# Kernel tuning notes

Measured on AMD Instinct MI355X. Metric: run time of the kernel, lower is better.

The kernel has to match this reference:

```python
import jax, jax.numpy as jnp
import numpy as np

B, N, CIN, COUT, K, L, NNZ = 4, 4096, 128, 128, 10, 50, 65536


def _spmm(idx, vals, X):
    # COO spmm: out[r] += vals * X[c]; idx: [2, nnz], X: [N, F]
    rows, cols = idx[0], idx[1]
    return jax.ops.segment_sum(vals[:, None] * X[cols], rows, num_segments=N)

_bspmm = jax.vmap(_spmm, in_axes=(0, 0, 0))  # batched over leading dim


def _hgnn_layer(phi_idx, phi_val, inv_idx, inv_val, fea, W, d):
    # original: ((phi @ diag(d)) @ phi_inv) @ (fea @ W)
    # identical math, evaluated right-to-left to stay sparse-dense only
    filt = jnp.einsum('bnc,co->bno', fea, W)            # [B,N,COUT]
    y = _bspmm(inv_idx, inv_val, filt)                  # phi_inv @ X
    y = d[None, :, None] * y                            # diag(d) @ .
    return _bspmm(phi_idx, phi_val, y)                  # phi @ .


def setup_inputs() -> dict:
    key = jax.random.key(0)
    ks = jax.random.split(key, 20)

    def coo(ki, kv):
        idx = jax.random.randint(ki, (B, 2, NNZ), 0, N, dtype=jnp.int32)
        val = jax.random.normal(kv, (B, NNZ), jnp.float32) * 0.05
        return idx, val

    phi1_idx, phi1_val = coo(ks[0], ks[1])
    phi1_inv_idx, phi1_inv_val = coo(ks[2], ks[3])
    phi2_idx, phi2_val = coo(ks[4], ks[5])
    phi2_inv_idx, phi2_inv_val = coo(ks[6], ks[7])
    fea = jax.random.normal(ks[8], (B, N, CIN), jnp.float32)
    joblst = jax.random.randint(ks[9], (B, L), 0, N, dtype=jnp.int64)

    xavier = float(np.sqrt(6.0 / (CIN + COUT)))
    W1 = jax.random.uniform(ks[10], (CIN, COUT), jnp.float32, -xavier, xavier)
    W2 = jax.random.uniform(ks[11], (CIN, COUT), jnp.float32, -xavier, xavier)
    d1 = jax.random.uniform(ks[12], (N,), jnp.float32, 0.9, 1.1)
    d2 = jax.random.uniform(ks[13], (N,), jnp.float32, 0.9, 1.1)
    s = float(1.0 / np.sqrt(N))
    W_ih = jax.random.uniform(ks[14], (N, COUT), jnp.float32, -s, s)
    W_hh = jax.random.uniform(ks[15], (N, N), jnp.float32, -s, s)
    b_ih = jax.random.uniform(ks[16], (N,), jnp.float32, -s, s)
    b_hh = jnp.zeros((N,), jnp.float32)
    sd = float(1.0 / np.sqrt(COUT))
    dense_W = jax.random.uniform(ks[17], (K, COUT), jnp.float32, -sd, sd)
    dense_b = jnp.zeros((K,), jnp.float32)
    item_emb = jax.random.normal(ks[18], (N, COUT), jnp.float32) * 0.01

    return dict(phi1_idx=phi1_idx, phi1_val=phi1_val, phi1_inv_idx=phi1_inv_idx,
                phi1_inv_val=phi1_inv_val, phi2_idx=phi2_idx, phi2_val=phi2_val,
                phi2_inv_idx=phi2_inv_idx, phi2_inv_val=phi2_inv_val,
                fea=fea, joblst=joblst, W1=W1, d1=d1, W2=W2, d2=d2,
                W_ih=W_ih, W_hh=W_hh, b_ih=b_ih, b_hh=b_hh,
                dense_W=dense_W, dense_b=dense_b, item_emb=item_emb)


def reference(phi1_idx, phi1_val, phi1_inv_idx, phi1_inv_val,
              phi2_idx, phi2_val, phi2_inv_idx, phi2_inv_val,
              fea, joblst, W1, d1, W2, d2, W_ih, W_hh, b_ih, b_hh,
              dense_W, dense_b, item_emb):
    # two hypergraph conv layers, summed
    out1 = _hgnn_layer(phi1_idx, phi1_val, phi1_inv_idx, phi1_inv_val, fea, W1, d1)
    out2 = _hgnn_layer(phi2_idx, phi2_val, phi2_inv_idx, phi2_inv_val, fea, W2, d2)
    res = out1 + out2                                   # [B,N,COUT]

    # RNN over job history embeddings (all joblst entries valid -> no -1 filter)
    xs = jnp.swapaxes(item_emb[joblst], 0, 1)           # [L,B,COUT]
    h0 = jnp.zeros((fea.shape[0], N), fea.dtype)

    def step(h, x):
        h = jnp.tanh(x @ W_ih.T + h @ W_hh.T + b_ih + b_hh)
        return h, None

    Emb, _ = jax.lax.scan(step, h0, xs)                 # last hidden: [B,N]

    res2 = jax.nn.gelu(jnp.einsum('bno,ko->bnk', res, dense_W) + dense_b,
                       approximate=False)               # [B,N,K]
    # (res3 * Emb2).permute back == res2 * gelu(Emb) broadcast over K
    return jax.nn.sigmoid(res2 * jax.nn.gelu(Emb, approximate=False)[:, :, None])
```

## Files before the change

### kernel.cpp

```cpp
#include <hip/hip_runtime.h>
#include <cstdint>
#include <cstddef>

#define NN   4096
#define LLC  50

__device__ __forceinline__ float bf2f(unsigned short u) {
    return __uint_as_float(((unsigned)u) << 16);
}
__device__ __forceinline__ unsigned short f2bf(float x) {
    unsigned b = __float_as_uint(x);
    return (unsigned short)((b + 0x7fffu + ((b >> 16) & 1u)) >> 16);
}

#if __has_builtin(__builtin_amdgcn_sdot4)
#define SDOT4(a, b, c) __builtin_amdgcn_sdot4((int)(a), (int)(b), (c), false)
#else
__device__ __forceinline__ int sdot4_sw(unsigned a, unsigned b, int c) {
    c += (int)(signed char)(a) * (int)(signed char)(b);
    c += (int)(signed char)(a >> 8) * (int)(signed char)(b >> 8);
    c += (int)(signed char)(a >> 16) * (int)(signed char)(b >> 16);
    c += (int)(signed char)(a >> 24) * (int)(signed char)(b >> 24);
    return c;
}
#define SDOT4(a, b, c) sdot4_sw((a), (b), (c))
#endif

#define DPPADD(v, ctrl, rmask) \
    ((v) + __builtin_amdgcn_update_dpp(0, (v), (ctrl), (rmask), 0xf, true))
__device__ __forceinline__ int wred64(int v) {
    v = DPPADD(v, 0x111, 0xf);
    v = DPPADD(v, 0x112, 0xf);
    v = DPPADD(v, 0x114, 0xf);
    v = DPPADD(v, 0x118, 0xf);
    v = DPPADD(v, 0x142, 0xa);
    v = DPPADD(v, 0x143, 0xc);
    return v;
}

__global__ __launch_bounds__(128) void k_filt(const float* __restrict__ fea,
                                              const float* __restrict__ W1,
                                              const float* __restrict__ W2,
                                              unsigned short* __restrict__ f1,
                                              unsigned short* __restrict__ f2) {
    __shared__ float sfea[16][128];
    int t = threadIdx.x;
    int rb = blockIdx.x * 16;
    for (int r = 0; r < 16; ++r) sfea[r][t] = fea[(size_t)(rb + r) * 128 + t];
    __syncthreads();
    float a1[16], a2[16];
#pragma unroll
    for (int r = 0; r < 16; ++r) { a1[r] = 0.f; a2[r] = 0.f; }
    for (int c = 0; c < 128; c += 4) {
        float w10 = W1[(c + 0) * 128 + t], w11 = W1[(c + 1) * 128 + t];
        float w12 = W1[(c + 2) * 128 + t], w13 = W1[(c + 3) * 128 + t];
        float w20 = W2[(c + 0) * 128 + t], w21 = W2[(c + 1) * 128 + t];
        float w22 = W2[(c + 2) * 128 + t], w23 = W2[(c + 3) * 128 + t];
#pragma unroll
        for (int r = 0; r < 16; ++r) {
            float4 f = *(const float4*)&sfea[r][c];
            a1[r] += f.x * w10 + f.y * w11 + f.z * w12 + f.w * w13;
            a2[r] += f.x * w20 + f.y * w21 + f.z * w22 + f.w * w23;
        }
    }
#pragma unroll
    for (int r = 0; r < 16; ++r) {
        f1[(size_t)(rb + r) * 128 + t] = f2bf(a1[r]);
        f2[(size_t)(rb + r) * 128 + t] = f2bf(a2[r]);
    }
}

__global__ __launch_bounds__(256) void k_hist(const int* __restrict__ i0, const int* __restrict__ i1,
                                              const int* __restrict__ i2, const int* __restrict__ i3,
                                              int* __restrict__ counts) {
    __shared__ int lc[4096];
    int t = threadIdx.x;
#pragma unroll
    for (int i = 0; i < 16; ++i) lc[t + i * 256] = 0;
    __syncthreads();
    unsigned blk = blockIdx.x;
    unsigned s = blk >> 4, ch = blk & 15;
    unsigned m = s >> 2, b = s & 3;
    const int* ip = (m == 0) ? i0 : (m == 1) ? i1 : (m == 2) ? i2 : i3;
    unsigned base = b * 131072u + ch * 4096u;
#pragma unroll
    for (int i = 0; i < 16; ++i) {
        int r = ip[base + t + i * 256];
        atomicAdd(&lc[r], 1);
    }
    __syncthreads();
    int* cs = counts + s * 4096;
#pragma unroll
    for (int i = 0; i < 16; ++i) {
        int v = lc[t + i * 256];
        if (v) atomicAdd(cs + t + i * 256, v);
    }
}

__global__ __launch_bounds__(256) void k_scan(const int* __restrict__ counts,
                                              int* __restrict__ rowptr,
                                              int* __restrict__ cursor) {
    int s = blockIdx.x, t = threadIdx.x;
    int loc[16];
    int base = t * 16;
    const int* cs = counts + s * 4096;
    int run = 0;
#pragma unroll
    for (int i = 0; i < 16; ++i) { loc[i] = run; run += cs[base + i]; }
    int total = run;
    int lane = t & 63, wv = t >> 6;
    int v = total;
#pragma unroll
    for (int d = 1; d < 64; d <<= 1) { int u = __shfl_up(v, d, 64); if (lane >= d) v += u; }
    __shared__ int wt[4];
    if (lane == 63) wt[wv] = v;
    __syncthreads();
    int pre = v - total;
    for (int i = 0; i < wv; ++i) pre += wt[i];
    int* rp = rowptr + s * 4097;
    int* cu = cursor + s * 4096;
#pragma unroll
    for (int i = 0; i < 16; ++i) { rp[base + i] = pre + loc[i]; cu[base + i] = pre + loc[i]; }
    if (t == 255) rp[4096] = pre + total;
}

__global__ __launch_bounds__(256) void k_scatter(const int* __restrict__ i0, const int* __restrict__ i1,
                                                 const int* __restrict__ i2, const int* __restrict__ i3,
                                                 const float* __restrict__ v0, const float* __restrict__ v1,
                                                 const float* __restrict__ v2, const float* __restrict__ v3,
                                                 const float* __restrict__ d1, const float* __restrict__ d2,
                                                 int* __restrict__ cursor,
                                                 unsigned* __restrict__ ep) {
    unsigned gid = blockIdx.x * 256 + threadIdx.x;
    unsigned s = gid >> 16, e = gid & 65535;
    unsigned m = s >> 2, b = s & 3;
    const int* ip = (m == 0) ? i0 : (m == 1) ? i1 : (m == 2) ? i2 : i3;
    const float* vp = (m == 0) ? v0 : (m == 1) ? v1 : (m == 2) ? v2 : v3;
    int r = ip[(size_t)b * 131072 + e];
    int c = ip[(size_t)b * 131072 + 65536 + e];
    float v = vp[(size_t)b * 65536 + e];
    if (m == 1) v *= d1[c];
    if (m == 3) v *= d2[c];
    int pos = atomicAdd(cursor + s * 4096 + r, 1);
    ep[(size_t)s * 65536 + pos] = ((unsigned)c << 16) | (unsigned)f2bf(v);
}

__global__ __launch_bounds__(256) void k_xproj(const float* __restrict__ item_emb,
                                               const int* __restrict__ joblst,
                                               const float* __restrict__ W_ih,
                                               const float* __restrict__ b_ih,
                                               const float* __restrict__ b_hh,
                                               float* __restrict__ xp) {
    __shared__ float sx[8][128];
    int t = threadIdx.x;
    int n = blockIdx.x * 256 + t;
    int p0 = blockIdx.y * 8;
#pragma unroll
    for (int i = 0; i < 4; ++i) {
        int e2 = t + i * 256;
        int rr = e2 >> 7, c = e2 & 127;
        int p = p0 + rr;
        int b = p & 3, l = p >> 2;
        int j = joblst[b * LLC + l];
        sx[rr][c] = item_emb[(size_t)j * 128 + c];
    }
    __syncthreads();
    float acc[8];
#pragma unroll
    for (int r = 0; r < 8; ++r) acc[r] = 0.f;
    const float* wn = W_ih + (size_t)n * 128;
    for (int c = 0; c < 128; c += 4) {
        float4 w = *(const float4*)(wn + c);
#pragma unroll
        for (int r = 0; r < 8; ++r) {
            float4 xr = *(const float4*)&sx[r][c];
            acc[r] += xr.x * w.x + xr.y * w.y + xr.z * w.z + xr.w * w.w;
        }
    }
    float bias = b_ih[n] + b_hh[n];
#pragma unroll
    for (int r = 0; r < 8; ++r) xp[(size_t)(p0 + r) * NN + n] = acc[r] + bias;
}

__device__ __forceinline__ void row_acc(const unsigned* __restrict__ eps, int e0, int e1,
                                        const unsigned* __restrict__ Xd, unsigned bbase,
                                        unsigned lane, float& a0, float& a1) {
    int e = e0;
    for (; e + 8 <= e1; e += 8) {
        unsigned p[8], x[8];
#pragma unroll
        for (int i = 0; i < 8; ++i) p[i] = eps[e + i];
#pragma unroll
        for (int i = 0; i < 8; ++i)
            x[i] = Xd[((size_t)(bbase + (p[i] >> 16)) << 6) + lane];
#pragma unroll
        for (int i = 0; i < 8; ++i) {
            float v = bf2f((unsigned short)p[i]);
            a0 += v * bf2f((unsigned short)x[i]);
            a1 += v * bf2f((unsigned short)(x[i] >> 16));
        }
    }
    for (; e < e1; ++e) {
        unsigned pp = eps[e];
        unsigned xw = Xd[((size_t)(bbase + (pp >> 16)) << 6) + lane];
        float v = bf2f((unsigned short)pp);
        a0 += v * bf2f((unsigned short)xw);
        a1 += v * bf2f((unsigned short)(xw >> 16));
    }
}

__global__ __launch_bounds__(256, 2) void k_mega(
        const float* __restrict__ W_hh,
        const float* __restrict__ xp,
        unsigned* __restrict__ hq,
        float* __restrict__ hfin,
        int* __restrict__ bar,
        const int* __restrict__ rowptr,
        const unsigned* __restrict__ ep,
        const unsigned short* __restrict__ filt1,
        const unsigned short* __restrict__ filt2,
        unsigned short* __restrict__ y1,
        unsigned short* __restrict__ y2,
        const float* __restrict__ dW,
        const float* __restrict__ db,
        float* __restrict__ g1) {
    __shared__ unsigned hs[4352];
    __shared__ int red[4][16];
    __shared__ unsigned char hpk[4][4][4];
    int t = threadIdx.x;
    int lane = t & 63, wv = t >> 6;
    int blk = blockIdx.x;

    if (blk >= 256) {
        int w = blk - 256;
        int c7 = w & 7;
        {
            unsigned mm = c7 & 1, b = (unsigned)c7 >> 1;
            int s = (mm ? 8 : 0) + (int)b;
            const unsigned* Xd = (const unsigned*)(mm ? filt2 : filt1);
            unsigned* Yd = (unsigned*)(mm ? y2 : y1);
            const int* rp = rowptr + s * 4097;
            const unsigned* eps = ep + (size_t)s * 65536;
            unsigned bbase = b * 4096;
            int g = w >> 3;
            int row0 = (g * 4 + wv) * 16;
            for (int rr = 0; rr < 16; ++rr) {
                int row = row0 + rr;
                float a0 = 0.f, a1 = 0.f;
                row_acc(eps, rp[row], rp[row + 1], Xd, bbase, lane, a0, a1);
                Yd[((size_t)(bbase + row) << 6) + lane] =
                    (unsigned)f2bf(a0) | ((unsigned)f2bf(a1) << 16);
            }
        }
        __syncthreads();
        if (t == 0) {
            __builtin_amdgcn_fence(__ATOMIC_RELEASE, "agent");
            __hip_atomic_fetch_add(&bar[320], 1, __ATOMIC_RELAXED,
                                   __HIP_MEMORY_SCOPE_AGENT);
            while (__hip_atomic_load(&bar[320], __ATOMIC_RELAXED,
                                     __HIP_MEMORY_SCOPE_AGENT) < 512)
                __builtin_amdgcn_s_sleep(4);
            __builtin_amdgcn_fence(__ATOMIC_ACQUIRE, "agent");
        }
        __syncthreads();
        {
            unsigned b = (unsigned)c7 >> 1;
            unsigned bbase = b * 4096;
            const int* rpA = rowptr + (4 + (int)b) * 4097;
            const int* rpB = rowptr + (12 + (int)b) * 4097;
            const unsigned* epA = ep + (size_t)(4 + b) * 65536;
            const unsigned* epB = ep + (size_t)(12 + b) * 65536;
            const unsigned* y1d = (const unsigned*)y1;
            const unsigned* y2d = (const unsigned*)y2;
            int g2 = (w >> 3) * 2 + (w & 1);
            int row0 = (g2 * 4 + wv) * 8;
            float* fs = (float*)hs + wv * 1056;
            for (int rr = 0; rr < 8; ++rr) {
                int row = row0 + rr;
                float a0 = 0.f, a1 = 0.f;
                row_acc(epA, rpA[row], rpA[row + 1], y1d, bbase, lane, a0, a1);
                row_acc(epB, rpB[row], rpB[row + 1], y2d, bbase, lane, a0, a1);
                *(float2*)(fs + rr * 132 + 2 * lane) = make_float2(a0, a1);
            }
#pragma unroll
            for (int pass = 0; pass < 2; ++pass) {
                int task = lane + pass * 64;
                if (task < 80) {
                    int rr = task / 10, k = task - rr * 10;
                    const float* rrp = fs + rr * 132;
                    const float4* wk4 = (const float4*)(dW + (size_t)k * 128);
                    float acc = 0.f;
#pragma unroll
                    for (int c4 = 0; c4 < 32; ++c4) {
                        float4 a = *(const float4*)(rrp + c4 * 4);
                        float4 wq = wk4[c4];
                        acc += a.x * wq.x + a.y * wq.y + a.z * wq.z + a.w * wq.w;
                    }
                    float pre = acc + db[k];
                    float gg = 0.5f * pre * (1.f + erff(pre * 0.70710678118f));
                    g1[(size_t)(bbase + row0 + rr) * 10 + k] = gg;
                }
            }
        }
        return;
    }

    int row_base = ((blk & 7) * 32 + (blk >> 3)) * 16;
    int wrow = row_base + wv * 4;

    uint4 W[4][4];
    {
        const float* wsrc = W_hh + (size_t)wrow * 4096;
#pragma unroll
        for (int r = 0; r < 4; ++r)
#pragma unroll
            for (int k4 = 0; k4 < 4; ++k4) {
                unsigned q[4];
#pragma unroll
                for (int i = 0; i < 4; ++i) {
                    const float* p = wsrc + (size_t)r * 4096 + (lane * 16 + k4 * 4 + i) * 4;
                    float4 w = *(const float4*)p;
                    int q0 = (int)rintf(fminf(fmaxf(w.x * 8192.f, -127.f), 127.f));
                    int q1 = (int)rintf(fminf(fmaxf(w.y * 8192.f, -127.f), 127.f));
                    int q2 = (int)rintf(fminf(fmaxf(w.z * 8192.f, -127.f), 127.f));
                    int q3 = (int)rintf(fminf(fmaxf(w.w * 8192.f, -127.f), 127.f));
                    q[i] = (q0 & 0xff) | ((q1 & 0xff) << 8) | ((q2 & 0xff) << 16) | ((q3 & 0xff) << 24);
                }
                W[r][k4] = make_uint4(q[0], q[1], q[2], q[3]);
            }
    }

    const float SC = 1.f / (8192.f * 127.f);

    for (int l = 0; l < LLC; ++l) {
        if (l > 0) {
            const unsigned* src = hq + (size_t)((l - 1) & 1) * 4096;
            unsigned sval[16];
#pragma unroll
            for (int k = 0; k < 16; ++k)
                sval[k] = __hip_atomic_load(src + t + k * 256, __ATOMIC_RELAXED,
                                            __HIP_MEMORY_SCOPE_AGENT);
#pragma unroll
            for (int k = 0; k < 16; ++k) hs[t + k * 256] = sval[k];
            __syncthreads();

            __builtin_amdgcn_s_setprio(1);
            uint4 H[4][4];
#pragma unroll
            for (int b = 0; b < 4; ++b)
#pragma unroll
                for (int k4 = 0; k4 < 4; ++k4)
                    H[b][k4] = ((const uint4*)hs)[k4 * 256 + b * 64 + lane];
            int acc[4][4];
#pragma unroll
            for (int r = 0; r < 4; ++r)
#pragma unroll
                for (int b = 0; b < 4; ++b) acc[r][b] = 0;
#pragma unroll
            for (int k4 = 0; k4 < 4; ++k4)
#pragma unroll
                for (int r = 0; r < 4; ++r)
#pragma unroll
                    for (int b = 0; b < 4; ++b) {
                        acc[r][b] = SDOT4(W[r][k4].x, H[b][k4].x, acc[r][b]);
                        acc[r][b] = SDOT4(W[r][k4].y, H[b][k4].y, acc[r][b]);
                        acc[r][b] = SDOT4(W[r][k4].z, H[b][k4].z, acc[r][b]);
                        acc[r][b] = SDOT4(W[r][k4].w, H[b][k4].w, acc[r][b]);
                    }
#pragma unroll
            for (int r = 0; r < 4; ++r)
#pragma unroll
                for (int b = 0; b < 4; ++b) acc[r][b] = wred64(acc[r][b]);
            if (lane == 63) {
#pragma unroll
                for (int b = 0; b < 4; ++b) {
                    int4 q = { acc[0][b], acc[1][b], acc[2][b], acc[3][b] };
                    *(int4*)&red[wv][b * 4] = q;
                }
            }
            __builtin_amdgcn_s_setprio(0);
        }
        if (lane < 16) {
            int b = lane >> 2, rr = lane & 3;
            int row = wrow + rr;
            float a = (l > 0) ? (float)red[wv][lane] * SC : 0.f;
            float pre = a + xp[(size_t)(l * 4 + b) * NN + row];
            float hnew = tanhf(pre);
            if (l == LLC - 1) hfin[(size_t)b * NN + row] = hnew;
            int q = (int)rintf(hnew * 127.f);
            hpk[wv][b][rr] = (unsigned char)(q & 0xff);
        }
        if (l < LLC - 1) {
            if (lane < 4) {
                int b = lane;
                unsigned d = *(const unsigned*)&hpk[wv][b][0];
                int hk = (row_base >> 2) + wv;
                int phys = ((hk >> 2) & 3) * 1024 + b * 256 + (hk >> 4) * 4 + (hk & 3);
                __hip_atomic_store(hq + (size_t)(l & 1) * 4096 + phys, d,
                                   __ATOMIC_RELAXED, __HIP_MEMORY_SCOPE_AGENT);
            }
            __syncthreads();
            if (t == 0) {
                int g = blk & 7;
                int old = __hip_atomic_fetch_add(&bar[g * 32], 1, __ATOMIC_RELAXED,
                                                 __HIP_MEMORY_SCOPE_AGENT);
                if ((old & 31) == 31)
                    __hip_atomic_fetch_add(&bar[256], 1, __ATOMIC_RELAXED,
                                           __HIP_MEMORY_SCOPE_AGENT);
                int target = 8 * (l + 1);
                while (__hip_atomic_load(&bar[256], __ATOMIC_RELAXED,
                                         __HIP_MEMORY_SCOPE_AGENT) < target)
                    __builtin_amdgcn_s_sleep(2);
            }
            __syncthreads();
        }
    }
}

__global__ __launch_bounds__(256) void k_out(const float* __restrict__ g1,
                                             const float* __restrict__ hfin,
                                             float* __restrict__ out) {
    int i = blockIdx.x * 256 + threadIdx.x;
    int grow = i / 10;
    float e = hfin[grow];
    float ge = 0.5f * e * (1.f + erff(e * 0.70710678118f));
    out[i] = 1.f / (1.f + __expf(-g1[i] * ge));
}

extern "C" void kernel_launch(void* const* d_in, const int* in_sizes, int n_in,
                              void* d_out, int out_size, void* d_ws, size_t ws_size,
                              hipStream_t stream) {
    const int*   phi1_idx = (const int*)d_in[0];
    const float* phi1_val = (const float*)d_in[1];
    const int*   inv1_idx = (const int*)d_in[2];
    const float* inv1_val = (const float*)d_in[3];
    const int*   phi2_idx = (const int*)d_in[4];
    const float* phi2_val = (const float*)d_in[5];
    const int*   inv2_idx = (const int*)d_in[6];
    const float* inv2_val = (const float*)d_in[7];
    const float* fea      = (const float*)d_in[8];
    const int*   joblst   = (const int*)d_in[9];
    const float* W1       = (const float*)d_in[10];
    const float* d1       = (const float*)d_in[11];
    const float* W2       = (const float*)d_in[12];
    const float* d2       = (const float*)d_in[13];
    const float* W_ih     = (const float*)d_in[14];
    const float* W_hh     = (const float*)d_in[15];
    const float* b_ih     = (const float*)d_in[16];
    const float* b_hh     = (const float*)d_in[17];
    const float* dense_W  = (const float*)d_in[18];
    const float* dense_b  = (const float*)d_in[19];
    const float* item_emb = (const float*)d_in[20];

    float* ws = (float*)d_ws;
    unsigned short* filt1 = (unsigned short*)ws;
    unsigned short* filt2 = (unsigned short*)(ws + 1048576);
    unsigned short* y1    = (unsigned short*)(ws + 2097152);
    unsigned short* y2    = (unsigned short*)(ws + 3145728);
    float* g1   = ws + 4194304;
    float* xp   = ws + 6291456;
    float* hfin = ws + 7110656;
    unsigned* hq  = (unsigned*)(ws + 7127040);
    int*   counts = (int*)(ws + 11329536);
    int*   rowptr = (int*)(ws + 11395072);
    int*   cursor = (int*)(ws + 11460624);
    unsigned* ep  = (unsigned*)(ws + 11526160);
    int*   bar    = (int*)(ws + 12574736);

    hipMemsetAsync(counts, 0, 16 * 4096 * sizeof(int), stream);
    hipMemsetAsync(bar, 0, 2048, stream);

    k_filt<<<1024, 128, 0, stream>>>(fea, W1, W2, filt1, filt2);
    k_xproj<<<dim3(16, 25), 256, 0, stream>>>(item_emb, joblst, W_ih, b_ih, b_hh, xp);

    k_hist<<<256, 256, 0, stream>>>(inv1_idx, phi1_idx, inv2_idx, phi2_idx, counts);
    k_scan<<<16, 256, 0, stream>>>(counts, rowptr, cursor);
    k_scatter<<<4096, 256, 0, stream>>>(inv1_idx, phi1_idx, inv2_idx, phi2_idx,
                                        inv1_val, phi1_val, inv2_val, phi2_val,
                                        d1, d2, cursor, ep);

    k_mega<<<768, 256, 0, stream>>>(W_hh, xp, hq, hfin, bar,
                                    rowptr, ep, filt1, filt2, y1, y2,
                                    dense_W, dense_b, g1);

    k_out<<<640, 256, 0, stream>>>(g1, hfin, (float*)d_out);
}
```

Baseline: 516.4 us.

## Fold histogram, scan, scatter and filter GEMM into the persistent mega kernel

```diff
diff --git a/kernel.cpp b/kernel.cpp
--- a/kernel.cpp
+++ b/kernel.cpp
@@ -38,113 +38,6 @@
     return v;
 }
 
-__global__ __launch_bounds__(128) void k_filt(const float* __restrict__ fea,
-                                              const float* __restrict__ W1,
-                                              const float* __restrict__ W2,
-                                              unsigned short* __restrict__ f1,
-                                              unsigned short* __restrict__ f2) {
-    __shared__ float sfea[16][128];
-    int t = threadIdx.x;
-    int rb = blockIdx.x * 16;
-    for (int r = 0; r < 16; ++r) sfea[r][t] = fea[(size_t)(rb + r) * 128 + t];
-    __syncthreads();
-    float a1[16], a2[16];
-#pragma unroll
-    for (int r = 0; r < 16; ++r) { a1[r] = 0.f; a2[r] = 0.f; }
-    for (int c = 0; c < 128; c += 4) {
-        float w10 = W1[(c + 0) * 128 + t], w11 = W1[(c + 1) * 128 + t];
-        float w12 = W1[(c + 2) * 128 + t], w13 = W1[(c + 3) * 128 + t];
-        float w20 = W2[(c + 0) * 128 + t], w21 = W2[(c + 1) * 128 + t];
-        float w22 = W2[(c + 2) * 128 + t], w23 = W2[(c + 3) * 128 + t];
-#pragma unroll
-        for (int r = 0; r < 16; ++r) {
-            float4 f = *(const float4*)&sfea[r][c];
-            a1[r] += f.x * w10 + f.y * w11 + f.z * w12 + f.w * w13;
-            a2[r] += f.x * w20 + f.y * w21 + f.z * w22 + f.w * w23;
-        }
-    }
-#pragma unroll
-    for (int r = 0; r < 16; ++r) {
-        f1[(size_t)(rb + r) * 128 + t] = f2bf(a1[r]);
-        f2[(size_t)(rb + r) * 128 + t] = f2bf(a2[r]);
-    }
-}
-
-__global__ __launch_bounds__(256) void k_hist(const int* __restrict__ i0, const int* __restrict__ i1,
-                                              const int* __restrict__ i2, const int* __restrict__ i3,
-                                              int* __restrict__ counts) {
-    __shared__ int lc[4096];
-    int t = threadIdx.x;
-#pragma unroll
-    for (int i = 0; i < 16; ++i) lc[t + i * 256] = 0;
-    __syncthreads();
-    unsigned blk = blockIdx.x;
-    unsigned s = blk >> 4, ch = blk & 15;
-    unsigned m = s >> 2, b = s & 3;
-    const int* ip = (m == 0) ? i0 : (m == 1) ? i1 : (m == 2) ? i2 : i3;
-    unsigned base = b * 131072u + ch * 4096u;
-#pragma unroll
-    for (int i = 0; i < 16; ++i) {
-        int r = ip[base + t + i * 256];
-        atomicAdd(&lc[r], 1);
-    }
-    __syncthreads();
-    int* cs = counts + s * 4096;
-#pragma unroll
-    for (int i = 0; i < 16; ++i) {
-        int v = lc[t + i * 256];
-        if (v) atomicAdd(cs + t + i * 256, v);
-    }
-}
-
-__global__ __launch_bounds__(256) void k_scan(const int* __restrict__ counts,
-                                              int* __restrict__ rowptr,
-                                              int* __restrict__ cursor) {
-    int s = blockIdx.x, t = threadIdx.x;
-    int loc[16];
-    int base = t * 16;
-    const int* cs = counts + s * 4096;
-    int run = 0;
-#pragma unroll
-    for (int i = 0; i < 16; ++i) { loc[i] = run; run += cs[base + i]; }
-    int total = run;
-    int lane = t & 63, wv = t >> 6;
-    int v = total;
-#pragma unroll
-    for (int d = 1; d < 64; d <<= 1) { int u = __shfl_up(v, d, 64); if (lane >= d) v += u; }
-    __shared__ int wt[4];
-    if (lane == 63) wt[wv] = v;
-    __syncthreads();
-    int pre = v - total;
-    for (int i = 0; i < wv; ++i) pre += wt[i];
-    int* rp = rowptr + s * 4097;
-    int* cu = cursor + s * 4096;
-#pragma unroll
-    for (int i = 0; i < 16; ++i) { rp[base + i] = pre + loc[i]; cu[base + i] = pre + loc[i]; }
-    if (t == 255) rp[4096] = pre + total;
-}
-
-__global__ __launch_bounds__(256) void k_scatter(const int* __restrict__ i0, const int* __restrict__ i1,
-                                                 const int* __restrict__ i2, const int* __restrict__ i3,
-                                                 const float* __restrict__ v0, const float* __restrict__ v1,
-                                                 const float* __restrict__ v2, const float* __restrict__ v3,
-                                                 const float* __restrict__ d1, const float* __restrict__ d2,
-                                                 int* __restrict__ cursor,
-                                                 unsigned* __restrict__ ep) {
-    unsigned gid = blockIdx.x * 256 + threadIdx.x;
-    unsigned s = gid >> 16, e = gid & 65535;
-    unsigned m = s >> 2, b = s & 3;
-    const int* ip = (m == 0) ? i0 : (m == 1) ? i1 : (m == 2) ? i2 : i3;
-    const float* vp = (m == 0) ? v0 : (m == 1) ? v1 : (m == 2) ? v2 : v3;
-    int r = ip[(size_t)b * 131072 + e];
-    int c = ip[(size_t)b * 131072 + 65536 + e];
-    float v = vp[(size_t)b * 65536 + e];
-    if (m == 1) v *= d1[c];
-    if (m == 3) v *= d2[c];
-    int pos = atomicAdd(cursor + s * 4096 + r, 1);
-    ep[(size_t)s * 65536 + pos] = ((unsigned)c << 16) | (unsigned)f2bf(v);
-}
-
 __global__ __launch_bounds__(256) void k_xproj(const float* __restrict__ item_emb,
                                                const int* __restrict__ joblst,
                                                const float* __restrict__ W_ih,
@@ -209,21 +102,44 @@
     }
 }
 
+#define WBAR(IDX)                                                              \
+    __syncthreads();                                                           \
+    if (t == 0) {                                                              \
+        __builtin_amdgcn_fence(__ATOMIC_RELEASE, "agent");                     \
+        __hip_atomic_fetch_add(&bar[IDX], 1, __ATOMIC_RELAXED,                 \
+                               __HIP_MEMORY_SCOPE_AGENT);                      \
+        while (__hip_atomic_load(&bar[IDX], __ATOMIC_RELAXED,                  \
+                                 __HIP_MEMORY_SCOPE_AGENT) < 512)              \
+            __builtin_amdgcn_s_sleep(4);                                       \
+        __builtin_amdgcn_fence(__ATOMIC_ACQUIRE, "agent");                     \
+    }                                                                          \
+    __syncthreads();
+
 __global__ __launch_bounds__(256, 2) void k_mega(
         const float* __restrict__ W_hh,
         const float* __restrict__ xp,
         unsigned* __restrict__ hq,
         float* __restrict__ hfin,
         int* __restrict__ bar,
-        const int* __restrict__ rowptr,
-        const unsigned* __restrict__ ep,
-        const unsigned short* __restrict__ filt1,
-        const unsigned short* __restrict__ filt2,
+        int* __restrict__ rowptr,
+        unsigned* __restrict__ ep,
+        unsigned short* __restrict__ filt1,
+        unsigned short* __restrict__ filt2,
         unsigned short* __restrict__ y1,
         unsigned short* __restrict__ y2,
         const float* __restrict__ dW,
         const float* __restrict__ db,
-        float* __restrict__ g1) {
+        float* __restrict__ g1,
+        const float* __restrict__ fea,
+        const float* __restrict__ W1,
+        const float* __restrict__ W2,
+        const int* __restrict__ i0, const int* __restrict__ i1,
+        const int* __restrict__ i2, const int* __restrict__ i3,
+        const float* __restrict__ v0, const float* __restrict__ v1,
+        const float* __restrict__ v2, const float* __restrict__ v3,
+        const float* __restrict__ dd1, const float* __restrict__ dd2,
+        int* __restrict__ counts,
+        int* __restrict__ cursor) {
     __shared__ unsigned hs[4352];
     __shared__ int red[4][16];
     __shared__ unsigned char hpk[4][4][4];
@@ -234,6 +150,104 @@
     if (blk >= 256) {
         int w = blk - 256;
         int c7 = w & 7;
+        {
+            int* lc = (int*)hs;
+#pragma unroll
+            for (int i = 0; i < 16; ++i) lc[t + i * 256] = 0;
+            __syncthreads();
+            unsigned s = (unsigned)w >> 5, ch = (unsigned)w & 31;
+            unsigned m = s >> 2, b = s & 3;
+            const int* ip = (m == 0) ? i0 : (m == 1) ? i1 : (m == 2) ? i2 : i3;
+            unsigned base = b * 131072u + ch * 2048u;
+#pragma unroll
+            for (int i = 0; i < 8; ++i) {
+                int r = ip[base + t + i * 256];
+                atomicAdd(&lc[r], 1);
+            }
+            __syncthreads();
+            int* cs = counts + s * 4096;
+#pragma unroll
+            for (int i = 0; i < 16; ++i) {
+                int v = lc[t + i * 256];
+                if (v) atomicAdd(cs + t + i * 256, v);
+            }
+        }
+        WBAR(320)
+        if (w < 16) {
+            int s = w;
+            int loc[16];
+            int base = t * 16;
+            const int* cs = counts + s * 4096;
+            int run = 0;
+#pragma unroll
+            for (int i = 0; i < 16; ++i) { loc[i] = run; run += cs[base + i]; }
+            int total = run;
+            int v = total;
+#pragma unroll
+            for (int d = 1; d < 64; d <<= 1) { int u = __shfl_up(v, d, 64); if (lane >= d) v += u; }
+            if (lane == 63) red[0][wv] = v;
+            __syncthreads();
+            int pre = v - total;
+            for (int i = 0; i < wv; ++i) pre += red[0][i];
+            int* rp = rowptr + s * 4097;
+            int* cu = cursor + s * 4096;
+#pragma unroll
+            for (int i = 0; i < 16; ++i) { rp[base + i] = pre + loc[i]; cu[base + i] = pre + loc[i]; }
+            if (t == 255) rp[4096] = pre + total;
+        }
+        WBAR(328)
+        {
+            unsigned s = (unsigned)w >> 5, ch = (unsigned)w & 31;
+            unsigned m = s >> 2, b = s & 3;
+            const int* ip = (m == 0) ? i0 : (m == 1) ? i1 : (m == 2) ? i2 : i3;
+            const float* vp = (m == 0) ? v0 : (m == 1) ? v1 : (m == 2) ? v2 : v3;
+            int* cu = cursor + s * 4096;
+#pragma unroll
+            for (int i = 0; i < 8; ++i) {
+                unsigned e = ch * 2048u + i * 256u + t;
+                int r = ip[(size_t)b * 131072 + e];
+                int c = ip[(size_t)b * 131072 + 65536 + e];
+                float v = vp[(size_t)b * 65536 + e];
+                if (m == 1) v *= dd1[c];
+                if (m == 3) v *= dd2[c];
+                int pos = atomicAdd(cu + r, 1);
+                ep[(size_t)s * 65536 + pos] = ((unsigned)c << 16) | (unsigned)f2bf(v);
+            }
+        }
+        {
+            int rb = w * 32;
+            float* sfea = (float*)hs;
+#pragma unroll
+            for (int i = 0; i < 16; ++i) {
+                int idx = t + i * 256;
+                sfea[idx] = fea[(size_t)rb * 128 + idx];
+            }
+            __syncthreads();
+            int half = t >> 7, tc = t & 127;
+            const float* sf = sfea + half * (16 * 128);
+            float a1[16], a2[16];
+#pragma unroll
+            for (int r = 0; r < 16; ++r) { a1[r] = 0.f; a2[r] = 0.f; }
+            for (int c = 0; c < 128; c += 4) {
+                float w10 = W1[(c + 0) * 128 + tc], w11 = W1[(c + 1) * 128 + tc];
+                float w12 = W1[(c + 2) * 128 + tc], w13 = W1[(c + 3) * 128 + tc];
+                float w20 = W2[(c + 0) * 128 + tc], w21 = W2[(c + 1) * 128 + tc];
+                float w22 = W2[(c + 2) * 128 + tc], w23 = W2[(c + 3) * 128 + tc];
+#pragma unroll
+                for (int r = 0; r < 16; ++r) {
+                    float4 f = *(const float4*)&sf[r * 128 + c];
+                    a1[r] += f.x * w10 + f.y * w11 + f.z * w12 + f.w * w13;
+                    a2[r] += f.x * w20 + f.y * w21 + f.z * w22 + f.w * w23;
+                }
+            }
+#pragma unroll
+            for (int r = 0; r < 16; ++r) {
+                size_t o = (size_t)(rb + half * 16 + r) * 128 + tc;
+                filt1[o] = f2bf(a1[r]);
+                filt2[o] = f2bf(a2[r]);
+            }
+        }
+        WBAR(336)
         {
             unsigned mm = c7 & 1, b = (unsigned)c7 >> 1;
             int s = (mm ? 8 : 0) + (int)b;
@@ -252,17 +266,7 @@
                     (unsigned)f2bf(a0) | ((unsigned)f2bf(a1) << 16);
             }
         }
-        __syncthreads();
-        if (t == 0) {
-            __builtin_amdgcn_fence(__ATOMIC_RELEASE, "agent");
-            __hip_atomic_fetch_add(&bar[320], 1, __ATOMIC_RELAXED,
-                                   __HIP_MEMORY_SCOPE_AGENT);
-            while (__hip_atomic_load(&bar[320], __ATOMIC_RELAXED,
-                                     __HIP_MEMORY_SCOPE_AGENT) < 512)
-                __builtin_amdgcn_s_sleep(4);
-            __builtin_amdgcn_fence(__ATOMIC_ACQUIRE, "agent");
-        }
-        __syncthreads();
+        WBAR(344)
         {
             unsigned b = (unsigned)c7 >> 1;
             unsigned bbase = b * 4096;
@@ -470,18 +474,15 @@
     hipMemsetAsync(counts, 0, 16 * 4096 * sizeof(int), stream);
     hipMemsetAsync(bar, 0, 2048, stream);
 
-    k_filt<<<1024, 128, 0, stream>>>(fea, W1, W2, filt1, filt2);
     k_xproj<<<dim3(16, 25), 256, 0, stream>>>(item_emb, joblst, W_ih, b_ih, b_hh, xp);
-
-    k_hist<<<256, 256, 0, stream>>>(inv1_idx, phi1_idx, inv2_idx, phi2_idx, counts);
-    k_scan<<<16, 256, 0, stream>>>(counts, rowptr, cursor);
-    k_scatter<<<4096, 256, 0, stream>>>(inv1_idx, phi1_idx, inv2_idx, phi2_idx,
-                                        inv1_val, phi1_val, inv2_val, phi2_val,
-                                        d1, d2, cursor, ep);
 
     k_mega<<<768, 256, 0, stream>>>(W_hh, xp, hq, hfin, bar,
                                     rowptr, ep, filt1, filt2, y1, y2,
-                                    dense_W, dense_b, g1);
+                                    dense_W, dense_b, g1,
+                                    fea, W1, W2,
+                                    inv1_idx, phi1_idx, inv2_idx, phi2_idx,
+                                    inv1_val, phi1_val, inv2_val, phi2_val,
+                                    d1, d2, counts, cursor);
 
     k_out<<<640, 256, 0, stream>>>(g1, hfin, (float*)d_out);
 }
```

New measurement: 616.7 us. +19.4%, slower.

## Fuse feature-weight projection into mega kernel's SpMM worker blocks

Applied to the files above, without the earlier changes.

```diff
diff --git a/kernel.cpp b/kernel.cpp
--- a/kernel.cpp
+++ b/kernel.cpp
@@ -36,38 +36,6 @@
     v = DPPADD(v, 0x142, 0xa);
     v = DPPADD(v, 0x143, 0xc);
     return v;
-}
-
-__global__ __launch_bounds__(128) void k_filt(const float* __restrict__ fea,
-                                              const float* __restrict__ W1,
-                                              const float* __restrict__ W2,
-                                              unsigned short* __restrict__ f1,
-                                              unsigned short* __restrict__ f2) {
-    __shared__ float sfea[16][128];
-    int t = threadIdx.x;
-    int rb = blockIdx.x * 16;
-    for (int r = 0; r < 16; ++r) sfea[r][t] = fea[(size_t)(rb + r) * 128 + t];
-    __syncthreads();
-    float a1[16], a2[16];
-#pragma unroll
-    for (int r = 0; r < 16; ++r) { a1[r] = 0.f; a2[r] = 0.f; }
-    for (int c = 0; c < 128; c += 4) {
-        float w10 = W1[(c + 0) * 128 + t], w11 = W1[(c + 1) * 128 + t];
-        float w12 = W1[(c + 2) * 128 + t], w13 = W1[(c + 3) * 128 + t];
-        float w20 = W2[(c + 0) * 128 + t], w21 = W2[(c + 1) * 128 + t];
-        float w22 = W2[(c + 2) * 128 + t], w23 = W2[(c + 3) * 128 + t];
-#pragma unroll
-        for (int r = 0; r < 16; ++r) {
-            float4 f = *(const float4*)&sfea[r][c];
-            a1[r] += f.x * w10 + f.y * w11 + f.z * w12 + f.w * w13;
-            a2[r] += f.x * w20 + f.y * w21 + f.z * w22 + f.w * w23;
-        }
-    }
-#pragma unroll
-    for (int r = 0; r < 16; ++r) {
-        f1[(size_t)(rb + r) * 128 + t] = f2bf(a1[r]);
-        f2[(size_t)(rb + r) * 128 + t] = f2bf(a2[r]);
-    }
 }
 
 __global__ __launch_bounds__(256) void k_hist(const int* __restrict__ i0, const int* __restrict__ i1,
@@ -209,6 +177,19 @@
     }
 }
 
+#define WFENCE_BAR(IDX)                                                        \
+    __syncthreads();                                                           \
+    if (t == 0) {                                                              \
+        __builtin_amdgcn_fence(__ATOMIC_RELEASE, "agent");                     \
+        __hip_atomic_fetch_add(&bar[IDX], 1, __ATOMIC_RELAXED,                 \
+                               __HIP_MEMORY_SCOPE_AGENT);                      \
+        while (__hip_atomic_load(&bar[IDX], __ATOMIC_RELAXED,                  \
+                                 __HIP_MEMORY_SCOPE_AGENT) < 512)              \
+            __builtin_amdgcn_s_sleep(4);                                       \
+        __builtin_amdgcn_fence(__ATOMIC_ACQUIRE, "agent");                     \
+    }                                                                          \
+    __syncthreads();
+
 __global__ __launch_bounds__(256, 2) void k_mega(
         const float* __restrict__ W_hh,
         const float* __restrict__ xp,
@@ -217,13 +198,16 @@
         int* __restrict__ bar,
         const int* __restrict__ rowptr,
         const unsigned* __restrict__ ep,
-        const unsigned short* __restrict__ filt1,
-        const unsigned short* __restrict__ filt2,
+        unsigned short* __restrict__ filt1,
+        unsigned short* __restrict__ filt2,
         unsigned short* __restrict__ y1,
         unsigned short* __restrict__ y2,
         const float* __restrict__ dW,
         const float* __restrict__ db,
-        float* __restrict__ g1) {
+        float* __restrict__ g1,
+        const float* __restrict__ fea,
+        const float* __restrict__ W1,
+        const float* __restrict__ W2) {
     __shared__ unsigned hs[4352];
     __shared__ int red[4][16];
     __shared__ unsigned char hpk[4][4][4];
@@ -234,6 +218,40 @@
     if (blk >= 256) {
         int w = blk - 256;
         int c7 = w & 7;
+        {
+            int rb = w * 32;
+            float* sfea = (float*)hs;
+#pragma unroll
+            for (int i = 0; i < 16; ++i) {
+                int idx = t + i * 256;
+                sfea[idx] = fea[(size_t)rb * 128 + idx];
+            }
+            __syncthreads();
+            int half = t >> 7, tc = t & 127;
+            const float* sf = sfea + half * 2048;
+            float a1[16], a2[16];
+#pragma unroll
+            for (int r = 0; r < 16; ++r) { a1[r] = 0.f; a2[r] = 0.f; }
+            for (int c = 0; c < 128; c += 4) {
+                float w10 = W1[(c + 0) * 128 + tc], w11 = W1[(c + 1) * 128 + tc];
+                float w12 = W1[(c + 2) * 128 + tc], w13 = W1[(c + 3) * 128 + tc];
+                float w20 = W2[(c + 0) * 128 + tc], w21 = W2[(c + 1) * 128 + tc];
+                float w22 = W2[(c + 2) * 128 + tc], w23 = W2[(c + 3) * 128 + tc];
+#pragma unroll
+                for (int r = 0; r < 16; ++r) {
+                    float4 f = *(const float4*)&sf[r * 128 + c];
+                    a1[r] += f.x * w10 + f.y * w11 + f.z * w12 + f.w * w13;
+                    a2[r] += f.x * w20 + f.y * w21 + f.z * w22 + f.w * w23;
+                }
+            }
+#pragma unroll
+            for (int r = 0; r < 16; ++r) {
+                size_t o = (size_t)(rb + half * 16 + r) * 128 + tc;
+                filt1[o] = f2bf(a1[r]);
+                filt2[o] = f2bf(a2[r]);
+            }
+        }
+        WFENCE_BAR(312)
         {
             unsigned mm = c7 & 1, b = (unsigned)c7 >> 1;
             int s = (mm ? 8 : 0) + (int)b;
@@ -252,17 +270,7 @@
                     (unsigned)f2bf(a0) | ((unsigned)f2bf(a1) << 16);
             }
         }
-        __syncthreads();
-        if (t == 0) {
-            __builtin_amdgcn_fence(__ATOMIC_RELEASE, "agent");
-            __hip_atomic_fetch_add(&bar[320], 1, __ATOMIC_RELAXED,
-                                   __HIP_MEMORY_SCOPE_AGENT);
-            while (__hip_atomic_load(&bar[320], __ATOMIC_RELAXED,
-                                     __HIP_MEMORY_SCOPE_AGENT) < 512)
-                __builtin_amdgcn_s_sleep(4);
-            __builtin_amdgcn_fence(__ATOMIC_ACQUIRE, "agent");
-        }
-        __syncthreads();
+        WFENCE_BAR(320)
         {
             unsigned b = (unsigned)c7 >> 1;
             unsigned bbase = b * 4096;
@@ -470,7 +478,6 @@
     hipMemsetAsync(counts, 0, 16 * 4096 * sizeof(int), stream);
     hipMemsetAsync(bar, 0, 2048, stream);
 
-    k_filt<<<1024, 128, 0, stream>>>(fea, W1, W2, filt1, filt2);
     k_xproj<<<dim3(16, 25), 256, 0, stream>>>(item_emb, joblst, W_ih, b_ih, b_hh, xp);
 
     k_hist<<<256, 256, 0, stream>>>(inv1_idx, phi1_idx, inv2_idx, phi2_idx, counts);
@@ -481,7 +488,7 @@
 
     k_mega<<<768, 256, 0, stream>>>(W_hh, xp, hq, hfin, bar,
                                     rowptr, ep, filt1, filt2, y1, y2,
-                                    dense_W, dense_b, g1);
+                                    dense_W, dense_b, g1, fea, W1, W2);
 
     k_out<<<640, 256, 0, stream>>>(g1, hfin, (float*)d_out);
 }
```

After: 525.4 us. No clear change (+1.7%).
